# Optimization experiments

Measured on AMD Instinct MI355X. Metric: run time of the kernel, lower is better.

## Reference

```python
import jax, jax.numpy as jnp
import numpy as np

# Config constants (match init_kwargs)
D_MODEL = 1024
D_MLP = 2048
NUM_EXPERTS = 8
EXPERTS_PER_TOKEN = 2
BATCH, SEQ = 2, 2048


def setup_inputs() -> dict:
    key = jax.random.key(0)
    k0, k1, k2, k3, k4 = jax.random.split(key, 5)
    init = lambda k, shape: jax.random.normal(k, shape, jnp.float32) * 0.02
    return {
        "x": jax.random.normal(k0, (BATCH, SEQ, D_MODEL), jnp.float32),
        "W_router": init(k1, (D_MODEL, NUM_EXPERTS)),
        "W_gate": init(k2, (NUM_EXPERTS, D_MODEL, D_MLP)),
        "W_in": init(k3, (NUM_EXPERTS, D_MODEL, D_MLP)),
        "W_out": init(k4, (NUM_EXPERTS, D_MLP, D_MODEL)),
    }


def reference(x, W_router, W_gate, W_in, W_out):
    B, S, D = x.shape
    h = x.reshape(-1, D)                                  # [T, D]
    T = h.shape[0]
    E = W_router.shape[1]

    # Router: softmax in fp32, top-k, renormalize (as in torch source)
    router_logits = h @ W_router                          # [T, E]
    probs = jax.nn.softmax(router_logits.astype(jnp.float32), axis=-1)
    top_w, top_i = jax.lax.top_k(probs, EXPERTS_PER_TOKEN)  # [T, K]
    top_w = top_w / top_w.sum(axis=-1, keepdims=True)
    top_w = top_w.astype(h.dtype)

    # Dense combine matrix [T, E]; top-k indices are distinct per token
    combine = jnp.zeros((T, E), h.dtype).at[jnp.arange(T)[:, None], top_i].set(top_w)

    # GatedMLP per expert: silu(h @ Wg) * (h @ Wi) @ Wo  (computed densely over experts,
    # then combined with the sparse routing weights -> same math as gather/MLP/scatter loop)
    gate_pre = jnp.einsum('td,edf->etf', h, W_gate)       # [E, T, F]
    up = jnp.einsum('td,edf->etf', h, W_in)               # [E, T, F]
    act = jax.nn.silu(gate_pre) * up                      # [E, T, F]
    expert_out = jnp.einsum('etf,efd->etd', act, W_out)   # [E, T, D]

    out = jnp.einsum('etd,te->td', expert_out, combine)   # [T, D]
    return out.reshape(B, S, D), router_logits
```

## Files before the change

### kernel.cpp

```cpp
#include <hip/hip_runtime.h>
#include <cstdint>
#include <cstddef>

#define T_TOK 4096
#define DM 1024
#define DF 2048
#define NE 8
#define PADROWS 9216
#define MAXTILES 72

typedef unsigned short u16;
typedef unsigned int u32;
using short8 = __attribute__((ext_vector_type(8))) short;
using f32x4  = __attribute__((ext_vector_type(4))) float;

static constexpr size_t OFF_H    = 0;
static constexpr size_t OFF_WGT  = OFF_H   + (size_t)T_TOK * DM * 2;
static constexpr size_t OFF_WIT  = OFF_WGT + (size_t)NE * DM * DF * 2;
static constexpr size_t OFF_WOT  = OFF_WIT + (size_t)NE * DM * DF * 2;
static constexpr size_t OFF_A    = OFF_WOT + (size_t)NE * DF * DM * 2;
static constexpr size_t OFF_TOK  = OFF_A   + (size_t)PADROWS * DF * 2;
static constexpr size_t OFF_WL   = OFF_TOK + PADROWS * 4;
static constexpr size_t OFF_TEXP = OFF_WL  + PADROWS * 4;
static constexpr size_t OFF_TW   = OFF_TEXP + (size_t)T_TOK * 2 * 4;
static constexpr size_t OFF_CNT  = OFF_TW  + (size_t)T_TOK * 2 * 4;
static constexpr size_t OFF_CUR  = OFF_CNT + 64;
static constexpr size_t OFF_NT   = OFF_CUR + 64;
static constexpr size_t OFF_TE   = OFF_NT  + 64;
static constexpr size_t OFF_TP   = OFF_TE  + 512;
static constexpr size_t OFF_ZPG  = OFF_TP  + 512;

__device__ __forceinline__ u16 f2bf(float f) {
  u32 u = __builtin_bit_cast(u32, f);
  u += 0x7FFFu + ((u >> 16) & 1u);
  return (u16)(u >> 16);
}

__device__ __forceinline__ void async16(const void* g, void* l) {
  __builtin_amdgcn_global_load_lds((__attribute__((address_space(1))) void*)(g),
                                   (__attribute__((address_space(3))) void*)(l),
                                   16, 0, 0);
}

__global__ void zero_out_k(float4* __restrict__ out) {
  out[(size_t)blockIdx.x * 256 + threadIdx.x] = make_float4(0.f, 0.f, 0.f, 0.f);
}

__global__ void convert_x_k(const float4* __restrict__ x, u16* __restrict__ h) {
  size_t i = (size_t)blockIdx.x * 256 + threadIdx.x;
  float4 v = x[i];
  u32 lo = (u32)f2bf(v.x) | ((u32)f2bf(v.y) << 16);
  u32 hi = (u32)f2bf(v.z) | ((u32)f2bf(v.w) << 16);
  uint2 o; o.x = lo; o.y = hi;
  *(uint2*)&h[i * 4] = o;
}

__global__ void init_small_k(int* __restrict__ tok, float* __restrict__ wl,
                             int* __restrict__ cnt, u16* __restrict__ zpg) {
  int i = blockIdx.x * 256 + threadIdx.x;
  if (i < PADROWS) { tok[i] = -1; wl[i] = 0.f; }
  if (i < NE) cnt[i] = 0;
  if (i < 2048) zpg[i] = 0;
}

__global__ void transpose_w_k(const float* __restrict__ Wg, const float* __restrict__ Wi,
                              const float* __restrict__ Wo, u16* __restrict__ wgT,
                              u16* __restrict__ wiT, u16* __restrict__ woT) {
  __shared__ u16 lT[64][65];
  int bid = blockIdx.x;
  int mat = bid >> 12;
  int r = bid & 4095;
  const float* src; u16* dst; int R, C;
  if (mat == 0)      { src = Wg; dst = wgT; R = DM; C = DF; }
  else if (mat == 1) { src = Wi; dst = wiT; R = DM; C = DF; }
  else               { src = Wo; dst = woT; R = DF; C = DM; }
  int e = r >> 9;
  int rem = r & 511;
  int ctiles = C >> 6;
  int tr = rem / ctiles, tc = rem % ctiles;
  size_t eb = (size_t)e * R * C;
  int r0 = tr * 64, c0 = tc * 64;
  int wv = threadIdx.x >> 6, lane = threadIdx.x & 63;
#pragma unroll
  for (int it = 0; it < 16; ++it) {
    int rl = it * 4 + wv;
    float v = src[eb + (size_t)(r0 + rl) * C + c0 + lane];
    lT[lane][rl] = f2bf(v);
  }
  __syncthreads();
#pragma unroll
  for (int it = 0; it < 16; ++it) {
    int cl = it * 4 + wv;
    dst[eb + (size_t)(c0 + cl) * R + r0 + lane] = lT[cl][lane];
  }
}

__global__ void router_k(const float* __restrict__ x, const float* __restrict__ Wr,
                         float* __restrict__ logits, int* __restrict__ texp,
                         float* __restrict__ tw, int* __restrict__ cnt) {
  int wv = threadIdx.x >> 6, lane = threadIdx.x & 63;
  int t = blockIdx.x * 4 + wv;
  const float* h = x + (size_t)t * DM;
  float acc[8] = {0.f, 0.f, 0.f, 0.f, 0.f, 0.f, 0.f, 0.f};
#pragma unroll
  for (int j = 0; j < 16; ++j) {
    float hv = h[lane + j * 64];
    const float4* wr = (const float4*)(Wr + (size_t)(lane + j * 64) * 8);
    float4 w0 = wr[0], w1 = wr[1];
    acc[0] += hv * w0.x; acc[1] += hv * w0.y; acc[2] += hv * w0.z; acc[3] += hv * w0.w;
    acc[4] += hv * w1.x; acc[5] += hv * w1.y; acc[6] += hv * w1.z; acc[7] += hv * w1.w;
  }
#pragma unroll
  for (int e = 0; e < 8; ++e)
#pragma unroll
    for (int off = 32; off > 0; off >>= 1) acc[e] += __shfl_down(acc[e], off, 64);
  if (lane == 0) {
    float mx = acc[0];
#pragma unroll
    for (int e = 1; e < 8; ++e) mx = fmaxf(mx, acc[e]);
    float p[8];
#pragma unroll
    for (int e = 0; e < 8; ++e) p[e] = __expf(acc[e] - mx);
    int i1 = 0; float b1 = p[0];
#pragma unroll
    for (int e = 1; e < 8; ++e) if (p[e] > b1) { b1 = p[e]; i1 = e; }
    int i2 = -1; float b2 = -1.f;
#pragma unroll
    for (int e = 0; e < 8; ++e) if (e != i1 && p[e] > b2) { b2 = p[e]; i2 = e; }
    float inv = 1.f / (b1 + b2);
    texp[t * 2] = i1; texp[t * 2 + 1] = i2;
    tw[t * 2] = b1 * inv; tw[t * 2 + 1] = b2 * inv;
    atomicAdd(&cnt[i1], 1); atomicAdd(&cnt[i2], 1);
#pragma unroll
    for (int e = 0; e < 8; ++e) logits[(size_t)t * 8 + e] = acc[e];
  }
}

__global__ void plan_k(const int* __restrict__ cnt, int* __restrict__ cursor,
                       int* __restrict__ tile_e, int* __restrict__ tile_p,
                       int* __restrict__ ntiles) {
  if (threadIdx.x == 0) {
    int off = 0, nt = 0;
    for (int e = 0; e < NE; ++e) {
      cursor[e] = off;
      int n = cnt[e];
      int t = (n + 127) >> 7;
      for (int i = 0; i < t; ++i) { tile_e[nt] = e; tile_p[nt] = off + i * 128; ++nt; }
      off += t * 128;
    }
    *ntiles = nt;
  }
}

__global__ void scatter_k(const int* __restrict__ texp, const float* __restrict__ tw,
                          int* __restrict__ cursor, int* __restrict__ tok,
                          float* __restrict__ wl) {
  int t = blockIdx.x * 256 + threadIdx.x;
#pragma unroll
  for (int k = 0; k < 2; ++k) {
    int e = texp[t * 2 + k];
    int p = atomicAdd(&cursor[e], 1);
    tok[p] = t;
    wl[p] = tw[t * 2 + k];
  }
}

__global__ __launch_bounds__(256) void gemm1_k(
    const u16* __restrict__ hbf, const u16* __restrict__ wgT, const u16* __restrict__ wiT,
    const int* __restrict__ tok, const float* __restrict__ wl,
    const int* __restrict__ tile_e, const int* __restrict__ tile_p,
    const int* __restrict__ ntiles, const u16* __restrict__ zpg,
    u16* __restrict__ Aact) {
  __shared__ u16 lH[128 * 64];
  __shared__ u16 lB[2][64 * 64];
  const int tile = blockIdx.y;
  if (tile >= *ntiles) return;
  const int e  = tile_e[tile];
  const int p0 = tile_p[tile];
  const int f0 = blockIdx.x * 64;
  const int tid = threadIdx.x, wv = tid >> 6, lane = tid & 63;

  const u16* hsrc[4];
  u16* hdst[4];
#pragma unroll
  for (int i = 0; i < 4; ++i) {
    const int row = wv * 32 + i * 8 + (lane >> 3);
    const int gc  = (lane & 7) ^ (row & 7);
    const int tk  = tok[p0 + row];
    hsrc[i] = (tk >= 0) ? (hbf + (size_t)tk * DM + gc * 8) : (zpg + gc * 8);
    hdst[i] = &lH[(wv * 32 + i * 8) * 64];
  }
  const u16* wbase = ((wv < 2) ? wgT : wiT) + (size_t)e * DM * DF;
  const int half = wv & 1, mt = wv >> 1;
  const u16* bsrc[4];
  u16* bdst[4];
#pragma unroll
  for (int i = 0; i < 4; ++i) {
    const int row = half * 32 + i * 8 + (lane >> 3);
    const int gc  = (lane & 7) ^ (row & 7);
    bsrc[i] = wbase + (size_t)(f0 + row) * DM + gc * 8;
    bdst[i] = &lB[mt][(half * 32 + i * 8) * 64];
  }

  f32x4 accG[4][2], accU[4][2];
#pragma unroll
  for (int m = 0; m < 4; ++m)
#pragma unroll
    for (int n = 0; n < 2; ++n) { accG[m][n] = (f32x4)(0.f); accU[m][n] = (f32x4)(0.f); }

  const int wr = wv >> 1, wc = wv & 1;
  const int wrBase = wr * 64, wcBase = wc * 32;
  const int l4 = lane >> 4, ln = lane & 15;

  for (int kt = 0; kt < DM / 64; ++kt) {
#pragma unroll
    for (int i = 0; i < 4; ++i) async16(hsrc[i] + (size_t)kt * 64, hdst[i]);
#pragma unroll
    for (int i = 0; i < 4; ++i) async16(bsrc[i] + (size_t)kt * 64, bdst[i]);
    __syncthreads();
#pragma unroll
    for (int s = 0; s < 2; ++s) {
      const int c = s * 4 + l4;
      short8 a[4], bg[2], bu[2];
#pragma unroll
      for (int m = 0; m < 4; ++m) {
        const int row = wrBase + m * 16 + ln;
        a[m] = *(const short8*)&lH[row * 64 + ((c ^ (row & 7)) * 8)];
      }
#pragma unroll
      for (int n = 0; n < 2; ++n) {
        const int rowb = wcBase + n * 16 + ln;
        const int off = rowb * 64 + ((c ^ (rowb & 7)) * 8);
        bg[n] = *(const short8*)&lB[0][off];
        bu[n] = *(const short8*)&lB[1][off];
      }
#pragma unroll
      for (int m = 0; m < 4; ++m)
#pragma unroll
        for (int n = 0; n < 2; ++n) {
          accG[m][n] = __builtin_amdgcn_mfma_f32_16x16x32_bf16(a[m], bg[n], accG[m][n], 0, 0, 0);
          accU[m][n] = __builtin_amdgcn_mfma_f32_16x16x32_bf16(a[m], bu[n], accU[m][n], 0, 0, 0);
        }
    }
    __syncthreads();
  }

#pragma unroll
  for (int m = 0; m < 4; ++m)
#pragma unroll
    for (int j = 0; j < 4; ++j) {
      const int row = wrBase + m * 16 + l4 * 4 + j;
      const int p = p0 + row;
      const float w = wl[p];
#pragma unroll
      for (int n = 0; n < 2; ++n) {
        const float g = accG[m][n][j];
        const float u = accU[m][n][j];
        const float val = (g / (1.f + __expf(-g))) * u * w;
        Aact[(size_t)p * DF + f0 + wcBase + n * 16 + ln] = f2bf(val);
      }
    }
}

__global__ __launch_bounds__(256) void gemm2_k(
    const u16* __restrict__ Aact, const u16* __restrict__ woT,
    const int* __restrict__ tok, const int* __restrict__ tile_e,
    const int* __restrict__ tile_p, const int* __restrict__ ntiles,
    float* __restrict__ out) {
  __shared__ u16 lA[128 * 64];
  __shared__ u16 lW[64 * 64];
  const int tile = blockIdx.y;
  if (tile >= *ntiles) return;
  const int e  = tile_e[tile];
  const int p0 = tile_p[tile];
  const int d0 = blockIdx.x * 64;
  const int tid = threadIdx.x, wv = tid >> 6, lane = tid & 63;

  const u16* asrc[4];
  u16* adst[4];
#pragma unroll
  for (int i = 0; i < 4; ++i) {
    const int row = wv * 32 + i * 8 + (lane >> 3);
    const int gc  = (lane & 7) ^ (row & 7);
    asrc[i] = Aact + (size_t)(p0 + row) * DF + gc * 8;
    adst[i] = &lA[(wv * 32 + i * 8) * 64];
  }
  const u16* wb = woT + (size_t)e * DM * DF;
  const u16* wsrc[2];
  u16* wdst[2];
#pragma unroll
  for (int i = 0; i < 2; ++i) {
    const int row = wv * 16 + i * 8 + (lane >> 3);
    const int gc  = (lane & 7) ^ (row & 7);
    wsrc[i] = wb + (size_t)(d0 + row) * DF + gc * 8;
    wdst[i] = &lW[(wv * 16 + i * 8) * 64];
  }

  f32x4 acc[4][2];
#pragma unroll
  for (int m = 0; m < 4; ++m)
#pragma unroll
    for (int n = 0; n < 2; ++n) acc[m][n] = (f32x4)(0.f);

  const int wr = wv >> 1, wc = wv & 1;
  const int wrBase = wr * 64, wcBase = wc * 32;
  const int l4 = lane >> 4, ln = lane & 15;

  for (int kt = 0; kt < DF / 64; ++kt) {
#pragma unroll
    for (int i = 0; i < 4; ++i) async16(asrc[i] + (size_t)kt * 64, adst[i]);
#pragma unroll
    for (int i = 0; i < 2; ++i) async16(wsrc[i] + (size_t)kt * 64, wdst[i]);
    __syncthreads();
#pragma unroll
    for (int s = 0; s < 2; ++s) {
      const int c = s * 4 + l4;
      short8 a[4], b[2];
#pragma unroll
      for (int m = 0; m < 4; ++m) {
        const int row = wrBase + m * 16 + ln;
        a[m] = *(const short8*)&lA[row * 64 + ((c ^ (row & 7)) * 8)];
      }
#pragma unroll
      for (int n = 0; n < 2; ++n) {
        const int rowb = wcBase + n * 16 + ln;
        b[n] = *(const short8*)&lW[rowb * 64 + ((c ^ (rowb & 7)) * 8)];
      }
#pragma unroll
      for (int m = 0; m < 4; ++m)
#pragma unroll
        for (int n = 0; n < 2; ++n)
          acc[m][n] = __builtin_amdgcn_mfma_f32_16x16x32_bf16(a[m], b[n], acc[m][n], 0, 0, 0);
    }
    __syncthreads();
  }

#pragma unroll
  for (int m = 0; m < 4; ++m)
#pragma unroll
    for (int j = 0; j < 4; ++j) {
      const int row = wrBase + m * 16 + l4 * 4 + j;
      const int p = p0 + row;
      const int tk = tok[p];
      if (tk >= 0) {
#pragma unroll
        for (int n = 0; n < 2; ++n) {
          atomicAdd(&out[(size_t)tk * DM + d0 + wcBase + n * 16 + ln], acc[m][n][j]);
        }
      }
    }
}

extern "C" void kernel_launch(void* const* d_in, const int* in_sizes, int n_in,
                              void* d_out, int out_size, void* d_ws, size_t ws_size,
                              hipStream_t stream) {
  const float* x  = (const float*)d_in[0];
  const float* Wr = (const float*)d_in[1];
  const float* Wg = (const float*)d_in[2];
  const float* Wi = (const float*)d_in[3];
  const float* Wo = (const float*)d_in[4];
  float* outF = (float*)d_out;
  float* logits = outF + (size_t)T_TOK * DM;

  char* ws = (char*)d_ws;
  u16*  hbf   = (u16*)(ws + OFF_H);
  u16*  wgT   = (u16*)(ws + OFF_WGT);
  u16*  wiT   = (u16*)(ws + OFF_WIT);
  u16*  woT   = (u16*)(ws + OFF_WOT);
  u16*  Aact  = (u16*)(ws + OFF_A);
  int*  tok   = (int*)(ws + OFF_TOK);
  float* wl   = (float*)(ws + OFF_WL);
  int*  texp  = (int*)(ws + OFF_TEXP);
  float* tw   = (float*)(ws + OFF_TW);
  int*  cnt   = (int*)(ws + OFF_CNT);
  int*  cur   = (int*)(ws + OFF_CUR);
  int*  nt    = (int*)(ws + OFF_NT);
  int*  te    = (int*)(ws + OFF_TE);
  int*  tp    = (int*)(ws + OFF_TP);
  u16*  zpg   = (u16*)(ws + OFF_ZPG);

  zero_out_k<<<4096, 256, 0, stream>>>((float4*)outF);
  convert_x_k<<<4096, 256, 0, stream>>>((const float4*)x, hbf);
  init_small_k<<<40, 256, 0, stream>>>(tok, wl, cnt, zpg);
  transpose_w_k<<<12288, 256, 0, stream>>>(Wg, Wi, Wo, wgT, wiT, woT);
  router_k<<<1024, 256, 0, stream>>>(x, Wr, logits, texp, tw, cnt);
  plan_k<<<1, 64, 0, stream>>>(cnt, cur, te, tp, nt);
  scatter_k<<<16, 256, 0, stream>>>(texp, tw, cur, tok, wl);
  gemm1_k<<<dim3(DF / 64, MAXTILES), 256, 0, stream>>>(hbf, wgT, wiT, tok, wl, te, tp, nt, zpg, Aact);
  gemm2_k<<<dim3(DM / 64, MAXTILES), 256, 0, stream>>>(Aact, woT, tok, te, tp, nt, outF);
}
```

Baseline: 393.8 us.

## Double-buffer MoE GEMM LDS tiles and replace atomic scatter with combine pass

Result: faster. 351.3 us (-10.8%).

```diff
diff --git a/kernel.cpp b/kernel.cpp
--- a/kernel.cpp
+++ b/kernel.cpp
@@ -29,6 +29,7 @@
 static constexpr size_t OFF_TE   = OFF_NT  + 64;
 static constexpr size_t OFF_TP   = OFF_TE  + 512;
 static constexpr size_t OFF_ZPG  = OFF_TP  + 512;
+static constexpr size_t OFF_POS  = OFF_ZPG + 4096;
 
 __device__ __forceinline__ u16 f2bf(float f) {
   u32 u = __builtin_bit_cast(u32, f);
@@ -40,10 +41,6 @@
   __builtin_amdgcn_global_load_lds((__attribute__((address_space(1))) void*)(g),
                                    (__attribute__((address_space(3))) void*)(l),
                                    16, 0, 0);
-}
-
-__global__ void zero_out_k(float4* __restrict__ out) {
-  out[(size_t)blockIdx.x * 256 + threadIdx.x] = make_float4(0.f, 0.f, 0.f, 0.f);
 }
 
 __global__ void convert_x_k(const float4* __restrict__ x, u16* __restrict__ h) {
@@ -154,7 +151,7 @@
 
 __global__ void scatter_k(const int* __restrict__ texp, const float* __restrict__ tw,
                           int* __restrict__ cursor, int* __restrict__ tok,
-                          float* __restrict__ wl) {
+                          float* __restrict__ wl, int* __restrict__ pos) {
   int t = blockIdx.x * 256 + threadIdx.x;
 #pragma unroll
   for (int k = 0; k < 2; ++k) {
@@ -162,6 +159,7 @@
     int p = atomicAdd(&cursor[e], 1);
     tok[p] = t;
     wl[p] = tw[t * 2 + k];
+    pos[t * 2 + k] = p;
   }
 }
 
@@ -171,8 +169,7 @@
     const int* __restrict__ tile_e, const int* __restrict__ tile_p,
     const int* __restrict__ ntiles, const u16* __restrict__ zpg,
     u16* __restrict__ Aact) {
-  __shared__ u16 lH[128 * 64];
-  __shared__ u16 lB[2][64 * 64];
+  __shared__ char smem[65536];
   const int tile = blockIdx.y;
   if (tile >= *ntiles) return;
   const int e  = tile_e[tile];
@@ -181,25 +178,25 @@
   const int tid = threadIdx.x, wv = tid >> 6, lane = tid & 63;
 
   const u16* hsrc[4];
-  u16* hdst[4];
+  int hoff[4];
 #pragma unroll
   for (int i = 0; i < 4; ++i) {
     const int row = wv * 32 + i * 8 + (lane >> 3);
     const int gc  = (lane & 7) ^ (row & 7);
     const int tk  = tok[p0 + row];
     hsrc[i] = (tk >= 0) ? (hbf + (size_t)tk * DM + gc * 8) : (zpg + gc * 8);
-    hdst[i] = &lH[(wv * 32 + i * 8) * 64];
+    hoff[i] = (wv * 32 + i * 8) * 64;
   }
   const u16* wbase = ((wv < 2) ? wgT : wiT) + (size_t)e * DM * DF;
   const int half = wv & 1, mt = wv >> 1;
   const u16* bsrc[4];
-  u16* bdst[4];
+  int boff[4];
 #pragma unroll
   for (int i = 0; i < 4; ++i) {
     const int row = half * 32 + i * 8 + (lane >> 3);
     const int gc  = (lane & 7) ^ (row & 7);
     bsrc[i] = wbase + (size_t)(f0 + row) * DM + gc * 8;
-    bdst[i] = &lB[mt][(half * 32 + i * 8) * 64];
+    boff[i] = 8192 + mt * 4096 + (half * 32 + i * 8) * 64;
   }
 
   f32x4 accG[4][2], accU[4][2];
@@ -212,12 +209,25 @@
   const int wrBase = wr * 64, wcBase = wc * 32;
   const int l4 = lane >> 4, ln = lane & 15;
 
+  {
+    u16* b = (u16*)smem;
+#pragma unroll
+    for (int i = 0; i < 4; ++i) async16(hsrc[i], b + hoff[i]);
+#pragma unroll
+    for (int i = 0; i < 4; ++i) async16(bsrc[i], b + boff[i]);
+  }
+  __syncthreads();
+
+  int cur = 0;
   for (int kt = 0; kt < DM / 64; ++kt) {
-#pragma unroll
-    for (int i = 0; i < 4; ++i) async16(hsrc[i] + (size_t)kt * 64, hdst[i]);
-#pragma unroll
-    for (int i = 0; i < 4; ++i) async16(bsrc[i] + (size_t)kt * 64, bdst[i]);
-    __syncthreads();
+    if (kt < DM / 64 - 1) {
+      u16* b = (u16*)smem + (cur ^ 1) * 16384;
+#pragma unroll
+      for (int i = 0; i < 4; ++i) async16(hsrc[i] + (size_t)(kt + 1) * 64, b + hoff[i]);
+#pragma unroll
+      for (int i = 0; i < 4; ++i) async16(bsrc[i] + (size_t)(kt + 1) * 64, b + boff[i]);
+    }
+    const u16* b = (const u16*)smem + cur * 16384;
 #pragma unroll
     for (int s = 0; s < 2; ++s) {
       const int c = s * 4 + l4;
@@ -225,14 +235,14 @@
 #pragma unroll
       for (int m = 0; m < 4; ++m) {
         const int row = wrBase + m * 16 + ln;
-        a[m] = *(const short8*)&lH[row * 64 + ((c ^ (row & 7)) * 8)];
+        a[m] = *(const short8*)&b[row * 64 + ((c ^ (row & 7)) * 8)];
       }
 #pragma unroll
       for (int n = 0; n < 2; ++n) {
         const int rowb = wcBase + n * 16 + ln;
-        const int off = rowb * 64 + ((c ^ (rowb & 7)) * 8);
-        bg[n] = *(const short8*)&lB[0][off];
-        bu[n] = *(const short8*)&lB[1][off];
+        const int so = rowb * 64 + ((c ^ (rowb & 7)) * 8);
+        bg[n] = *(const short8*)&b[8192 + so];
+        bu[n] = *(const short8*)&b[12288 + so];
       }
 #pragma unroll
       for (int m = 0; m < 4; ++m)
@@ -243,32 +253,38 @@
         }
     }
     __syncthreads();
-  }
-
+    cur ^= 1;
+  }
+
+  u16* lOut = (u16*)smem;
 #pragma unroll
   for (int m = 0; m < 4; ++m)
 #pragma unroll
     for (int j = 0; j < 4; ++j) {
       const int row = wrBase + m * 16 + l4 * 4 + j;
-      const int p = p0 + row;
-      const float w = wl[p];
+      const float w = wl[p0 + row];
 #pragma unroll
       for (int n = 0; n < 2; ++n) {
         const float g = accG[m][n][j];
         const float u = accU[m][n][j];
         const float val = (g / (1.f + __expf(-g))) * u * w;
-        Aact[(size_t)p * DF + f0 + wcBase + n * 16 + ln] = f2bf(val);
+        lOut[row * 80 + wcBase + n * 16 + ln] = f2bf(val);
       }
     }
+  __syncthreads();
+  const int r = tid >> 1, hf = tid & 1;
+  u16* gdst = Aact + (size_t)(p0 + r) * DF + f0 + hf * 32;
+  const u16* lsrc = &lOut[r * 80 + hf * 32];
+#pragma unroll
+  for (int i = 0; i < 4; ++i)
+    *(short8*)(gdst + i * 8) = *(const short8*)(lsrc + i * 8);
 }
 
 __global__ __launch_bounds__(256) void gemm2_k(
     const u16* __restrict__ Aact, const u16* __restrict__ woT,
-    const int* __restrict__ tok, const int* __restrict__ tile_e,
-    const int* __restrict__ tile_p, const int* __restrict__ ntiles,
-    float* __restrict__ out) {
-  __shared__ u16 lA[128 * 64];
-  __shared__ u16 lW[64 * 64];
+    const int* __restrict__ tile_e, const int* __restrict__ tile_p,
+    const int* __restrict__ ntiles, float* __restrict__ scr) {
+  __shared__ char smem[49152];
   const int tile = blockIdx.y;
   if (tile >= *ntiles) return;
   const int e  = tile_e[tile];
@@ -277,23 +293,23 @@
   const int tid = threadIdx.x, wv = tid >> 6, lane = tid & 63;
 
   const u16* asrc[4];
-  u16* adst[4];
+  int aoff[4];
 #pragma unroll
   for (int i = 0; i < 4; ++i) {
     const int row = wv * 32 + i * 8 + (lane >> 3);
     const int gc  = (lane & 7) ^ (row & 7);
     asrc[i] = Aact + (size_t)(p0 + row) * DF + gc * 8;
-    adst[i] = &lA[(wv * 32 + i * 8) * 64];
+    aoff[i] = (wv * 32 + i * 8) * 64;
   }
   const u16* wb = woT + (size_t)e * DM * DF;
   const u16* wsrc[2];
-  u16* wdst[2];
+  int woff[2];
 #pragma unroll
   for (int i = 0; i < 2; ++i) {
     const int row = wv * 16 + i * 8 + (lane >> 3);
     const int gc  = (lane & 7) ^ (row & 7);
     wsrc[i] = wb + (size_t)(d0 + row) * DF + gc * 8;
-    wdst[i] = &lW[(wv * 16 + i * 8) * 64];
+    woff[i] = 8192 + (wv * 16 + i * 8) * 64;
   }
 
   f32x4 acc[4][2];
@@ -306,33 +322,47 @@
   const int wrBase = wr * 64, wcBase = wc * 32;
   const int l4 = lane >> 4, ln = lane & 15;
 
+  {
+    u16* b = (u16*)smem;
+#pragma unroll
+    for (int i = 0; i < 4; ++i) async16(asrc[i], b + aoff[i]);
+#pragma unroll
+    for (int i = 0; i < 2; ++i) async16(wsrc[i], b + woff[i]);
+  }
+  __syncthreads();
+
+  int cur = 0;
   for (int kt = 0; kt < DF / 64; ++kt) {
-#pragma unroll
-    for (int i = 0; i < 4; ++i) async16(asrc[i] + (size_t)kt * 64, adst[i]);
-#pragma unroll
-    for (int i = 0; i < 2; ++i) async16(wsrc[i] + (size_t)kt * 64, wdst[i]);
-    __syncthreads();
+    if (kt < DF / 64 - 1) {
+      u16* b = (u16*)smem + (cur ^ 1) * 12288;
+#pragma unroll
+      for (int i = 0; i < 4; ++i) async16(asrc[i] + (size_t)(kt + 1) * 64, b + aoff[i]);
+#pragma unroll
+      for (int i = 0; i < 2; ++i) async16(wsrc[i] + (size_t)(kt + 1) * 64, b + woff[i]);
+    }
+    const u16* b = (const u16*)smem + cur * 12288;
 #pragma unroll
     for (int s = 0; s < 2; ++s) {
       const int c = s * 4 + l4;
-      short8 a[4], b[2];
+      short8 a[4], bw[2];
 #pragma unroll
       for (int m = 0; m < 4; ++m) {
         const int row = wrBase + m * 16 + ln;
-        a[m] = *(const short8*)&lA[row * 64 + ((c ^ (row & 7)) * 8)];
+        a[m] = *(const short8*)&b[row * 64 + ((c ^ (row & 7)) * 8)];
       }
 #pragma unroll
       for (int n = 0; n < 2; ++n) {
         const int rowb = wcBase + n * 16 + ln;
-        b[n] = *(const short8*)&lW[rowb * 64 + ((c ^ (rowb & 7)) * 8)];
+        bw[n] = *(const short8*)&b[8192 + rowb * 64 + ((c ^ (rowb & 7)) * 8)];
       }
 #pragma unroll
       for (int m = 0; m < 4; ++m)
 #pragma unroll
         for (int n = 0; n < 2; ++n)
-          acc[m][n] = __builtin_amdgcn_mfma_f32_16x16x32_bf16(a[m], b[n], acc[m][n], 0, 0, 0);
+          acc[m][n] = __builtin_amdgcn_mfma_f32_16x16x32_bf16(a[m], bw[n], acc[m][n], 0, 0, 0);
     }
     __syncthreads();
+    cur ^= 1;
   }
 
 #pragma unroll
@@ -340,15 +370,23 @@
 #pragma unroll
     for (int j = 0; j < 4; ++j) {
       const int row = wrBase + m * 16 + l4 * 4 + j;
-      const int p = p0 + row;
-      const int tk = tok[p];
-      if (tk >= 0) {
-#pragma unroll
-        for (int n = 0; n < 2; ++n) {
-          atomicAdd(&out[(size_t)tk * DM + d0 + wcBase + n * 16 + ln], acc[m][n][j]);
-        }
-      }
-    }
+      float* dst = scr + (size_t)(p0 + row) * DM + d0;
+#pragma unroll
+      for (int n = 0; n < 2; ++n)
+        dst[wcBase + n * 16 + ln] = acc[m][n][j];
+    }
+}
+
+__global__ void combine_k(const float* __restrict__ scr, const int* __restrict__ pos,
+                          float* __restrict__ out) {
+  const int t = blockIdx.x;
+  const int d = threadIdx.x;
+  const int p1 = pos[t * 2], p2 = pos[t * 2 + 1];
+  const float4 a = *(const float4*)(scr + (size_t)p1 * DM + d * 4);
+  const float4 b = *(const float4*)(scr + (size_t)p2 * DM + d * 4);
+  float4 o;
+  o.x = a.x + b.x; o.y = a.y + b.y; o.z = a.z + b.z; o.w = a.w + b.w;
+  *(float4*)(out + (size_t)t * DM + d * 4) = o;
 }
 
 extern "C" void kernel_launch(void* const* d_in, const int* in_sizes, int n_in,
@@ -378,14 +416,16 @@
   int*  te    = (int*)(ws + OFF_TE);
   int*  tp    = (int*)(ws + OFF_TP);
   u16*  zpg   = (u16*)(ws + OFF_ZPG);
-
-  zero_out_k<<<4096, 256, 0, stream>>>((float4*)outF);
+  int*  pos   = (int*)(ws + OFF_POS);
+  float* scr  = (float*)(ws + OFF_WGT);
+
   convert_x_k<<<4096, 256, 0, stream>>>((const float4*)x, hbf);
   init_small_k<<<40, 256, 0, stream>>>(tok, wl, cnt, zpg);
   transpose_w_k<<<12288, 256, 0, stream>>>(Wg, Wi, Wo, wgT, wiT, woT);
   router_k<<<1024, 256, 0, stream>>>(x, Wr, logits, texp, tw, cnt);
   plan_k<<<1, 64, 0, stream>>>(cnt, cur, te, tp, nt);
-  scatter_k<<<16, 256, 0, stream>>>(texp, tw, cur, tok, wl);
+  scatter_k<<<16, 256, 0, stream>>>(texp, tw, cur, tok, wl, pos);
   gemm1_k<<<dim3(DF / 64, MAXTILES), 256, 0, stream>>>(hbf, wgT, wiT, tok, wl, te, tp, nt, zpg, Aact);
-  gemm2_k<<<dim3(DM / 64, MAXTILES), 256, 0, stream>>>(Aact, woT, tok, te, tp, nt, outF);
-}
+  gemm2_k<<<dim3(DM / 64, MAXTILES), 256, 0, stream>>>(Aact, woT, te, tp, nt, scr);
+  combine_k<<<4096, 256, 0, stream>>>(scr, pos, outF);
+}
```
